# Optimization experiments

Measured on AMD Instinct MI355X. Metric: run time of the kernel, lower is better.

Reference implementation:

```python
import jax, jax.numpy as jnp
import numpy as np

NEG_INF = -jnp.inf  # aggregation identity for the max-plus semifield


def setup_inputs() -> dict:
    key = jax.random.key(0)
    k1, k2, k3 = jax.random.split(key, 3)
    B, C_in, C_out, H, W, M, N = 4, 32, 32, 80, 80, 5, 5
    x = jax.random.normal(k1, (B, C_in, H, W), dtype=jnp.float32)
    w = jax.random.normal(k2, (C_out, C_in, M, N), dtype=jnp.float32) * 0.1
    bias = jax.random.normal(k3, (C_out,), dtype=jnp.float32) * 0.1
    return {"x": x, "w": w, "bias": bias}


def reference(x, w, bias):
    """Max-plus semifield conv: out[b,co,h,w] = bias[co] + sum_ci max_{m,n} (x_pad[b,ci,h+m,w+n] + w[co,ci,m,n]).

    Faithful to SemiConv2d._semi_conv with semifield = (amax, add, -inf, 0),
    but computed with a running max over the MN taps instead of materializing
    the [B, C_out, C_in, M*N, H*W] tensor the torch code builds via unfold.
    """
    B, C_in, H, W = x.shape
    C_out, _, M, N = w.shape
    # padding exactly as in _semi_conv (odd vs even kernel), fill = aggregation identity
    pt, pb = (M // 2, M // 2) if M % 2 else (M // 2 - 1, M // 2)
    pl, pr = (N // 2, N // 2) if N % 2 else (N // 2 - 1, N // 2)
    xp = jnp.pad(x, ((0, 0), (0, 0), (pt, pb), (pl, pr)), constant_values=NEG_INF)
    # running max over the M*N taps (fixed small loop, not a data-dim loop)
    acc = jnp.full((B, C_out, C_in, H, W), NEG_INF, dtype=x.dtype)
    for m in range(M):
        for n in range(N):
            patch = xp[:, :, m:m + H, n:n + W]               # [B, C_in, H, W]
            tap = patch[:, None] + w[None, :, :, m, n, None, None]  # [B, C_out, C_in, H, W]
            acc = jnp.maximum(acc, tap)
    out = jnp.sum(acc, axis=2) + bias[None, :, None, None]   # sum over C_in, add bias
    return out
```

## Files before the change

kernel.cpp:

```cpp
#include <hip/hip_runtime.h>
#include <math.h>

#define CIN  32
#define COUT 32
#define BB   4
#define HH   80
#define WW   80
#define HW   (HH * WW)
#define NOUT (BB * COUT * HW)
#define TH   16
#define XR   20
#define XC   88
#define TILE (XR * XC)
#define NT   320

typedef float v4f __attribute__((ext_vector_type(4)));

__device__ __forceinline__ float max3f(float a, float b, float c) {
    float d;
    asm("v_max3_f32 %0, %1, %2, %3" : "=v"(d) : "v"(a), "v"(b), "v"(c));
    return d;
}

__device__ __forceinline__ void load_lds4(const float* g, float* l) {
    __builtin_amdgcn_global_load_lds(
        (const __attribute__((address_space(1))) void*)g,
        (__attribute__((address_space(3))) void*)l, 4, 0, 0);
}

template<int NP>
__global__ __launch_bounds__(NT, 6) void semiconv_kernel(
    const float* __restrict__ x,
    const float* __restrict__ w,
    float* __restrict__ dst)
{
    constexpr int CP = CIN / NP;
    __shared__ __align__(16) float xs[CP][TILE];
    __shared__ __align__(16) float wl[CP * 100];

    const int tid = threadIdx.x;
    const int bh  = blockIdx.x;
    const int cq  = blockIdx.y;
    const int zz  = blockIdx.z;
    const int b    = zz / NP;
    const int part = zz % NP;
    const int ci0  = part * CP;
    const int h0   = bh * TH;
    const int co0  = cq * 4;

    const int ty = tid / 20, tx = tid % 20, wc = tx * 4;
    const int xro = ty * XC + wc;

    int goff[6];
    #pragma unroll
    for (int i = 0; i < 6; ++i) {
        int idx = tid + i * NT;
        int r = idx / XC, c = idx % XC;
        int gr = h0 + r - 2, gc = c - 2;
        bool in = (idx < TILE) && gr >= 0 && gr < HH && gc >= 0 && gc < WW;
        goff[i] = in ? (gr * WW + gc) : -1;
    }
    const bool has6 = (tid < TILE - 5 * NT);

    const float* xb0 = x + (size_t)(b * CIN + ci0) * HW;
    const int wave64 = tid & ~63;
    #pragma unroll
    for (int t = 0; t < CP; ++t) {
        const float* xp = xb0 + (size_t)t * HW;
        #pragma unroll
        for (int i = 0; i < 5; ++i)
            if (goff[i] >= 0) load_lds4(xp + goff[i], &xs[t][i * NT + wave64]);
        if (has6 && goff[5] >= 0) load_lds4(xp + goff[5], &xs[t][5 * NT + wave64]);
    }

    for (int idx = tid; idx < CP * 100; idx += NT) {
        int cop = idx / (CP * 25);
        int r   = idx % (CP * 25);
        int k = r / 25, t = r % 25, m = t / 5, n = t % 5;
        wl[k * 100 + m * 20 + n * 4 + cop] =
            w[((size_t)(co0 + cop) * CIN + ci0) * 25 + r];
    }

    #pragma unroll
    for (int i = 0; i < 6; ++i) {
        int idx = tid + i * NT;
        if (idx < TILE && goff[i] < 0) {
            #pragma unroll
            for (int t = 0; t < CP; ++t) xs[t][idx] = -INFINITY;
        }
    }

    float s[4][4];
    #pragma unroll
    for (int c = 0; c < 4; ++c)
        #pragma unroll
        for (int j = 0; j < 4; ++j) s[c][j] = 0.f;

    __syncthreads();

    #pragma unroll
    for (int k = 0; k < CP; ++k) {
        const float* xb = &xs[k][xro];
        const float* wk = &wl[k * 100];
        float acc[4][4];
        #pragma unroll
        for (int m = 0; m < 5; ++m) {
            v4f A  = *(const v4f*)(xb + m * XC);
            v4f C  = *(const v4f*)(xb + m * XC + 4);
            v4f W0 = *(const v4f*)(wk + m * 20);
            v4f W1 = *(const v4f*)(wk + m * 20 + 4);
            v4f W2 = *(const v4f*)(wk + m * 20 + 8);
            v4f W3 = *(const v4f*)(wk + m * 20 + 12);
            v4f W4 = *(const v4f*)(wk + m * 20 + 16);
            float xr[8] = {A.x, A.y, A.z, A.w, C.x, C.y, C.z, C.w};
            #pragma unroll
            for (int c = 0; c < 4; ++c) {
                float q0 = W0[c], q1 = W1[c], q2 = W2[c], q3 = W3[c], q4 = W4[c];
                #pragma unroll
                for (int j = 0; j < 4; ++j) {
                    float t = max3f(xr[j] + q0, xr[j + 1] + q1, xr[j + 2] + q2);
                    float u = fmaxf(xr[j + 3] + q3, xr[j + 4] + q4);
                    acc[c][j] = (m == 0) ? fmaxf(t, u) : max3f(acc[c][j], t, u);
                }
            }
        }
        #pragma unroll
        for (int c = 0; c < 4; ++c)
            #pragma unroll
            for (int j = 0; j < 4; ++j) s[c][j] += acc[c][j];
    }

    size_t oi = (((size_t)b * COUT + co0) * HH + (h0 + ty)) * WW + wc;
    float* o = dst + (size_t)part * NOUT;
    #pragma unroll
    for (int c = 0; c < 4; ++c) {
        v4f r = {s[c][0], s[c][1], s[c][2], s[c][3]};
        *(v4f*)(o + oi + (size_t)c * HW) = r;
    }
}

template<int NP>
__global__ __launch_bounds__(256) void reduceN_kernel(
    const float* __restrict__ ws, const float* __restrict__ bias,
    float* __restrict__ out)
{
    int i4 = blockIdx.x * 256 + threadIdx.x;
    const float4* p = reinterpret_cast<const float4*>(ws);
    float4 r = p[i4];
    #pragma unroll
    for (int q = 1; q < NP; ++q) {
        float4 t = p[i4 + (size_t)q * (NOUT / 4)];
        r.x += t.x; r.y += t.y; r.z += t.z; r.w += t.w;
    }
    int co = (i4 / (HW / 4)) & (COUT - 1);
    float bc = bias[co];
    r.x += bc; r.y += bc; r.z += bc; r.w += bc;
    reinterpret_cast<float4*>(out)[i4] = r;
}

__global__ __launch_bounds__(256) void naive_kernel(
    const float* __restrict__ x, const float* __restrict__ w,
    const float* __restrict__ bias, float* __restrict__ out)
{
    int o = blockIdx.x * 256 + threadIdx.x;
    if (o >= NOUT) return;
    int wcol = o % WW, h = (o / WW) % HH, co = (o / HW) % COUT, b = o / (COUT * HW);
    float sum = 0.f;
    for (int ci = 0; ci < CIN; ++ci) {
        float mx = -INFINITY;
        for (int m = 0; m < 5; ++m) {
            int gr = h + m - 2;
            if (gr < 0 || gr >= HH) continue;
            for (int n = 0; n < 5; ++n) {
                int gc = wcol + n - 2;
                if (gc < 0 || gc >= WW) continue;
                float v = x[((size_t)(b * CIN + ci)) * HW + gr * WW + gc]
                        + w[((size_t)(co * CIN + ci)) * 25 + m * 5 + n];
                mx = fmaxf(mx, v);
            }
        }
        sum += mx;
    }
    out[o] = sum + bias[co];
}

extern "C" void kernel_launch(void* const* d_in, const int* in_sizes, int n_in,
                              void* d_out, int out_size, void* d_ws, size_t ws_size,
                              hipStream_t stream) {
    const float* x    = (const float*)d_in[0];
    const float* w    = (const float*)d_in[1];
    const float* bias = (const float*)d_in[2];
    float* out        = (float*)d_out;

    const size_t need8 = 8ull * NOUT * sizeof(float);
    const size_t need4 = 4ull * NOUT * sizeof(float);

    if (ws_size >= need8) {
        dim3 grid(HH / TH, COUT / 4, BB * 8);
        semiconv_kernel<8><<<grid, NT, 0, stream>>>(x, w, (float*)d_ws);
        reduceN_kernel<8><<<NOUT / 4 / 256, 256, 0, stream>>>((const float*)d_ws, bias, out);
    } else if (ws_size >= need4) {
        dim3 grid(HH / TH, COUT / 4, BB * 4);
        semiconv_kernel<4><<<grid, NT, 0, stream>>>(x, w, (float*)d_ws);
        reduceN_kernel<4><<<NOUT / 4 / 256, 256, 0, stream>>>((const float*)d_ws, bias, out);
    } else {
        naive_kernel<<<(NOUT + 255) / 256, 256, 0, stream>>>(x, w, bias, out);
    }
}
```

Measured before the change: 42.79 us.

## Remap threads to one output channel by 8 rows, reusing input rows across taps

New measurement: 51.16 us. 19.6% more time.

```diff
diff --git a/kernel.cpp b/kernel.cpp
--- a/kernel.cpp
+++ b/kernel.cpp
@@ -29,27 +29,29 @@
 }
 
 template<int NP>
-__global__ __launch_bounds__(NT, 6) void semiconv_kernel(
+__global__ __launch_bounds__(NT, 4) void semiconv_kernel(
     const float* __restrict__ x,
     const float* __restrict__ w,
     float* __restrict__ dst)
 {
     constexpr int CP = CIN / NP;
-    __shared__ __align__(16) float xs[CP][TILE];
-    __shared__ __align__(16) float wl[CP * 100];
+    __shared__ __align__(16) float xs[CP * TILE];
+    __shared__ __align__(16) float wl[CP * 8 * 40];
 
     const int tid = threadIdx.x;
     const int bh  = blockIdx.x;
-    const int cq  = blockIdx.y;
+    const int cg  = blockIdx.y;
     const int zz  = blockIdx.z;
     const int b    = zz / NP;
     const int part = zz % NP;
     const int ci0  = part * CP;
     const int h0   = bh * TH;
-    const int co0  = cq * 4;
-
-    const int ty = tid / 20, tx = tid % 20, wc = tx * 4;
-    const int xro = ty * XC + wc;
+    const int co0  = cg * 8;
+
+    const int co_t = tid / 40;
+    const int rem  = tid % 40;
+    const int rg   = rem / 20;
+    const int cgx  = rem % 20;
 
     int goff[6];
     #pragma unroll
@@ -67,18 +69,19 @@
     #pragma unroll
     for (int t = 0; t < CP; ++t) {
         const float* xp = xb0 + (size_t)t * HW;
+        float* xd = xs + t * TILE;
         #pragma unroll
         for (int i = 0; i < 5; ++i)
-            if (goff[i] >= 0) load_lds4(xp + goff[i], &xs[t][i * NT + wave64]);
-        if (has6 && goff[5] >= 0) load_lds4(xp + goff[5], &xs[t][5 * NT + wave64]);
-    }
-
-    for (int idx = tid; idx < CP * 100; idx += NT) {
-        int cop = idx / (CP * 25);
-        int r   = idx % (CP * 25);
-        int k = r / 25, t = r % 25, m = t / 5, n = t % 5;
-        wl[k * 100 + m * 20 + n * 4 + cop] =
-            w[((size_t)(co0 + cop) * CIN + ci0) * 25 + r];
+            if (goff[i] >= 0) load_lds4(xp + goff[i], xd + i * NT + wave64);
+        if (has6 && goff[5] >= 0) load_lds4(xp + goff[5], xd + 5 * NT + wave64);
+    }
+
+    for (int idx = tid; idx < CP * 320; idx += NT) {
+        int n = idx & 7, t = idx >> 3;
+        int m = t % 5, u = t / 5;
+        int cop = u & 7, k = u >> 3;
+        wl[idx] = (n < 5)
+            ? w[((size_t)(co0 + cop) * CIN + ci0 + k) * 25 + m * 5 + n] : 0.0f;
     }
 
     #pragma unroll
@@ -86,56 +89,67 @@
         int idx = tid + i * NT;
         if (idx < TILE && goff[i] < 0) {
             #pragma unroll
-            for (int t = 0; t < CP; ++t) xs[t][idx] = -INFINITY;
-        }
-    }
-
-    float s[4][4];
-    #pragma unroll
-    for (int c = 0; c < 4; ++c)
-        #pragma unroll
-        for (int j = 0; j < 4; ++j) s[c][j] = 0.f;
+            for (int t = 0; t < CP; ++t) xs[t * TILE + idx] = -INFINITY;
+        }
+    }
+
+    float s[8][4];
+    #pragma unroll
+    for (int r = 0; r < 8; ++r)
+        #pragma unroll
+        for (int j = 0; j < 4; ++j) s[r][j] = 0.f;
+
+    const int xoff = rg * 8 * XC + cgx * 4;
+    const int woff = co_t * 40;
 
     __syncthreads();
 
-    #pragma unroll
+    #pragma unroll 1
     for (int k = 0; k < CP; ++k) {
-        const float* xb = &xs[k][xro];
-        const float* wk = &wl[k * 100];
-        float acc[4][4];
+        const float* xk = xs + k * TILE + xoff;
+        const float* wk = wl + k * 320 + woff;
+
+        float wm[5][5];
         #pragma unroll
         for (int m = 0; m < 5; ++m) {
-            v4f A  = *(const v4f*)(xb + m * XC);
-            v4f C  = *(const v4f*)(xb + m * XC + 4);
-            v4f W0 = *(const v4f*)(wk + m * 20);
-            v4f W1 = *(const v4f*)(wk + m * 20 + 4);
-            v4f W2 = *(const v4f*)(wk + m * 20 + 8);
-            v4f W3 = *(const v4f*)(wk + m * 20 + 12);
-            v4f W4 = *(const v4f*)(wk + m * 20 + 16);
+            v4f W0 = *(const v4f*)(wk + m * 8);
+            v4f W1 = *(const v4f*)(wk + m * 8 + 4);
+            wm[m][0] = W0.x; wm[m][1] = W0.y; wm[m][2] = W0.z;
+            wm[m][3] = W0.w; wm[m][4] = W1.x;
+        }
+
+        float acc[8][4];
+        #pragma unroll
+        for (int rho = 0; rho < 12; ++rho) {
+            v4f A = *(const v4f*)(xk + rho * XC);
+            v4f C = *(const v4f*)(xk + rho * XC + 4);
             float xr[8] = {A.x, A.y, A.z, A.w, C.x, C.y, C.z, C.w};
             #pragma unroll
-            for (int c = 0; c < 4; ++c) {
-                float q0 = W0[c], q1 = W1[c], q2 = W2[c], q3 = W3[c], q4 = W4[c];
+            for (int m = 0; m < 5; ++m) {
+                const int r = rho - m;
+                if (r < 0 || r > 7) continue;
                 #pragma unroll
                 for (int j = 0; j < 4; ++j) {
-                    float t = max3f(xr[j] + q0, xr[j + 1] + q1, xr[j + 2] + q2);
-                    float u = fmaxf(xr[j + 3] + q3, xr[j + 4] + q4);
-                    acc[c][j] = (m == 0) ? fmaxf(t, u) : max3f(acc[c][j], t, u);
+                    float t = max3f(xr[j] + wm[m][0], xr[j + 1] + wm[m][1],
+                                    xr[j + 2] + wm[m][2]);
+                    float u = fmaxf(xr[j + 3] + wm[m][3], xr[j + 4] + wm[m][4]);
+                    acc[r][j] = (m == 0) ? fmaxf(t, u) : max3f(acc[r][j], t, u);
                 }
             }
         }
         #pragma unroll
-        for (int c = 0; c < 4; ++c)
+        for (int r = 0; r < 8; ++r)
             #pragma unroll
-            for (int j = 0; j < 4; ++j) s[c][j] += acc[c][j];
-    }
-
-    size_t oi = (((size_t)b * COUT + co0) * HH + (h0 + ty)) * WW + wc;
-    float* o = dst + (size_t)part * NOUT;
-    #pragma unroll
-    for (int c = 0; c < 4; ++c) {
-        v4f r = {s[c][0], s[c][1], s[c][2], s[c][3]};
-        *(v4f*)(o + oi + (size_t)c * HW) = r;
+            for (int j = 0; j < 4; ++j) s[r][j] += acc[r][j];
+    }
+
+    float* o = dst + (size_t)part * NOUT
+             + (((size_t)b * COUT + co0 + co_t) * HH + (h0 + rg * 8)) * WW
+             + cgx * 4;
+    #pragma unroll
+    for (int r = 0; r < 8; ++r) {
+        v4f v = {s[r][0], s[r][1], s[r][2], s[r][3]};
+        *(v4f*)(o + r * WW) = v;
     }
 }
 
@@ -196,11 +210,11 @@
     const size_t need4 = 4ull * NOUT * sizeof(float);
 
     if (ws_size >= need8) {
-        dim3 grid(HH / TH, COUT / 4, BB * 8);
+        dim3 grid(HH / TH, COUT / 8, BB * 8);
         semiconv_kernel<8><<<grid, NT, 0, stream>>>(x, w, (float*)d_ws);
         reduceN_kernel<8><<<NOUT / 4 / 256, 256, 0, stream>>>((const float*)d_ws, bias, out);
     } else if (ws_size >= need4) {
-        dim3 grid(HH / TH, COUT / 4, BB * 4);
+        dim3 grid(HH / TH, COUT / 8, BB * 4);
         semiconv_kernel<4><<<grid, NT, 0, stream>>>(x, w, (float*)d_ws);
         reduceN_kernel<4><<<NOUT / 4 / 256, 256, 0, stream>>>((const float*)d_ws, bias, out);
     } else {
```

## Assign one output channel per wave with 20-wide column strips per thread

Applied to the files above, without the earlier changes.

New measurement: 43.90 us. 1.03x slower.

```diff
diff --git a/kernel.cpp b/kernel.cpp
--- a/kernel.cpp
+++ b/kernel.cpp
@@ -12,7 +12,7 @@
 #define XR   20
 #define XC   88
 #define TILE (XR * XC)
-#define NT   320
+#define NT   512
 
 typedef float v4f __attribute__((ext_vector_type(4)));
 
@@ -29,60 +29,51 @@
 }
 
 template<int NP>
-__global__ __launch_bounds__(NT, 6) void semiconv_kernel(
+__global__ __launch_bounds__(NT, 4) void semiconv_kernel(
     const float* __restrict__ x,
     const float* __restrict__ w,
     float* __restrict__ dst)
 {
     constexpr int CP = CIN / NP;
     __shared__ __align__(16) float xs[CP][TILE];
-    __shared__ __align__(16) float wl[CP * 100];
 
     const int tid = threadIdx.x;
     const int bh  = blockIdx.x;
-    const int cq  = blockIdx.y;
+    const int cog = blockIdx.y;
     const int zz  = blockIdx.z;
     const int b    = zz / NP;
     const int part = zz % NP;
     const int ci0  = part * CP;
     const int h0   = bh * TH;
-    const int co0  = cq * 4;
 
-    const int ty = tid / 20, tx = tid % 20, wc = tx * 4;
-    const int xro = ty * XC + wc;
+    const int wave = __builtin_amdgcn_readfirstlane(tid >> 6);
+    const int lane = tid & 63;
+    const int co   = cog * 8 + wave;
+    const int r    = lane >> 2;
+    const int g    = lane & 3;
 
-    int goff[6];
+    int goff[4];
     #pragma unroll
-    for (int i = 0; i < 6; ++i) {
+    for (int i = 0; i < 4; ++i) {
         int idx = tid + i * NT;
-        int r = idx / XC, c = idx % XC;
-        int gr = h0 + r - 2, gc = c - 2;
+        int rr = idx / XC, cc = idx % XC;
+        int gr = h0 + rr - 2, gc = cc - 2;
         bool in = (idx < TILE) && gr >= 0 && gr < HH && gc >= 0 && gc < WW;
         goff[i] = in ? (gr * WW + gc) : -1;
     }
-    const bool has6 = (tid < TILE - 5 * NT);
 
     const float* xb0 = x + (size_t)(b * CIN + ci0) * HW;
-    const int wave64 = tid & ~63;
+    const int wbase = wave * 64;
     #pragma unroll
     for (int t = 0; t < CP; ++t) {
         const float* xp = xb0 + (size_t)t * HW;
         #pragma unroll
-        for (int i = 0; i < 5; ++i)
-            if (goff[i] >= 0) load_lds4(xp + goff[i], &xs[t][i * NT + wave64]);
-        if (has6 && goff[5] >= 0) load_lds4(xp + goff[5], &xs[t][5 * NT + wave64]);
-    }
-
-    for (int idx = tid; idx < CP * 100; idx += NT) {
-        int cop = idx / (CP * 25);
-        int r   = idx % (CP * 25);
-        int k = r / 25, t = r % 25, m = t / 5, n = t % 5;
-        wl[k * 100 + m * 20 + n * 4 + cop] =
-            w[((size_t)(co0 + cop) * CIN + ci0) * 25 + r];
+        for (int i = 0; i < 4; ++i)
+            if (goff[i] >= 0) load_lds4(xp + goff[i], &xs[t][i * NT + wbase]);
     }
 
     #pragma unroll
-    for (int i = 0; i < 6; ++i) {
+    for (int i = 0; i < 4; ++i) {
         int idx = tid + i * NT;
         if (idx < TILE && goff[i] < 0) {
             #pragma unroll
@@ -90,52 +81,51 @@
         }
     }
 
-    float s[4][4];
+    const float* wp = w + (size_t)(co * CIN + ci0) * 25;
+
+    float s[20];
     #pragma unroll
-    for (int c = 0; c < 4; ++c)
-        #pragma unroll
-        for (int j = 0; j < 4; ++j) s[c][j] = 0.f;
+    for (int j = 0; j < 20; ++j) s[j] = 0.f;
 
     __syncthreads();
 
-    #pragma unroll
+    #pragma unroll 1
     for (int k = 0; k < CP; ++k) {
-        const float* xb = &xs[k][xro];
-        const float* wk = &wl[k * 100];
-        float acc[4][4];
+        float wk[25];
+        #pragma unroll
+        for (int j = 0; j < 25; ++j) wk[j] = wp[k * 25 + j];
+
+        const float* xk = &xs[k][r * XC + 20 * g];
+        float acc[20];
         #pragma unroll
         for (int m = 0; m < 5; ++m) {
-            v4f A  = *(const v4f*)(xb + m * XC);
-            v4f C  = *(const v4f*)(xb + m * XC + 4);
-            v4f W0 = *(const v4f*)(wk + m * 20);
-            v4f W1 = *(const v4f*)(wk + m * 20 + 4);
-            v4f W2 = *(const v4f*)(wk + m * 20 + 8);
-            v4f W3 = *(const v4f*)(wk + m * 20 + 12);
-            v4f W4 = *(const v4f*)(wk + m * 20 + 16);
-            float xr[8] = {A.x, A.y, A.z, A.w, C.x, C.y, C.z, C.w};
+            const float* xrow = xk + m * XC;
+            float F[24];
             #pragma unroll
-            for (int c = 0; c < 4; ++c) {
-                float q0 = W0[c], q1 = W1[c], q2 = W2[c], q3 = W3[c], q4 = W4[c];
-                #pragma unroll
-                for (int j = 0; j < 4; ++j) {
-                    float t = max3f(xr[j] + q0, xr[j + 1] + q1, xr[j + 2] + q2);
-                    float u = fmaxf(xr[j + 3] + q3, xr[j + 4] + q4);
-                    acc[c][j] = (m == 0) ? fmaxf(t, u) : max3f(acc[c][j], t, u);
-                }
+            for (int t = 0; t < 6; ++t) {
+                v4f v = *(const v4f*)(xrow + 4 * t);
+                F[4*t] = v.x; F[4*t+1] = v.y; F[4*t+2] = v.z; F[4*t+3] = v.w;
+            }
+            #pragma unroll
+            for (int j = 0; j < 20; ++j) {
+                float t1 = max3f(F[j]     + wk[5*m],
+                                 F[j + 1] + wk[5*m + 1],
+                                 F[j + 2] + wk[5*m + 2]);
+                float t2 = fmaxf(F[j + 3] + wk[5*m + 3],
+                                 F[j + 4] + wk[5*m + 4]);
+                acc[j] = (m == 0) ? fmaxf(t1, t2) : max3f(acc[j], t1, t2);
             }
         }
         #pragma unroll
-        for (int c = 0; c < 4; ++c)
-            #pragma unroll
-            for (int j = 0; j < 4; ++j) s[c][j] += acc[c][j];
+        for (int j = 0; j < 20; ++j) s[j] += acc[j];
     }
 
-    size_t oi = (((size_t)b * COUT + co0) * HH + (h0 + ty)) * WW + wc;
-    float* o = dst + (size_t)part * NOUT;
+    float* o = dst + (size_t)part * NOUT
+             + (((size_t)b * COUT + co) * HH + (h0 + r)) * WW + 20 * g;
     #pragma unroll
-    for (int c = 0; c < 4; ++c) {
-        v4f r = {s[c][0], s[c][1], s[c][2], s[c][3]};
-        *(v4f*)(o + oi + (size_t)c * HW) = r;
+    for (int t = 0; t < 5; ++t) {
+        v4f v = {s[4*t], s[4*t+1], s[4*t+2], s[4*t+3]};
+        *(v4f*)(o + 4 * t) = v;
     }
 }
 
@@ -196,11 +186,11 @@
     const size_t need4 = 4ull * NOUT * sizeof(float);
 
     if (ws_size >= need8) {
-        dim3 grid(HH / TH, COUT / 4, BB * 8);
+        dim3 grid(HH / TH, COUT / 8, BB * 8);
         semiconv_kernel<8><<<grid, NT, 0, stream>>>(x, w, (float*)d_ws);
         reduceN_kernel<8><<<NOUT / 4 / 256, 256, 0, stream>>>((const float*)d_ws, bias, out);
     } else if (ws_size >= need4) {
-        dim3 grid(HH / TH, COUT / 4, BB * 4);
+        dim3 grid(HH / TH, COUT / 8, BB * 4);
         semiconv_kernel<4><<<grid, NT, 0, stream>>>(x, w, (float*)d_ws);
         reduceN_kernel<4><<<NOUT / 4 / 256, 256, 0, stream>>>((const float*)d_ws, bias, out);
     } else {
```
